# Performance work log

Measured on AMD Instinct MI355X. Metric: run time of the kernel, lower is better.

The kernel has to match this reference:

```python
import jax, jax.numpy as jnp
import numpy as np

N = 100000      # number of vertices
E = 3200000     # number of directed edges (avg degree 32)
EPS = 1e-8
WEIGHT = 0.01


def setup_inputs() -> dict:
    key = jax.random.key(0)
    k1, k2, k3, k4 = jax.random.split(key, 4)
    mu0 = jax.random.normal(k1, (N, 3), dtype=jnp.float32)
    # current positions = canonical + small deformation (realistic ARAP setting)
    mu = mu0 + 0.1 * jax.random.normal(k2, (N, 3), dtype=jnp.float32)
    i = jax.random.randint(k3, (E,), 0, N, dtype=jnp.int32)
    # avoid self-edges (rest length 0 would give w = 1/eps = 1e8 and swamp the loss)
    off = jax.random.randint(k4, (E,), 1, N, dtype=jnp.int32)
    j = (i + off) % N
    edge_idx = jnp.stack([i, j], axis=0)  # (2, E)
    return {"mu0": mu0, "mu": mu, "edge_idx": edge_idx}


def reference(mu0, mu, edge_idx):
    i, j = edge_idx[0], edge_idx[1]
    rest = mu0[j] - mu0[i]        # (E,3) canonical edge vectors
    deform = mu[j] - mu[i]        # (E,3) deformed edge vectors
    w = 1.0 / (jnp.linalg.norm(rest, axis=-1) + EPS)  # (E,)
    # per-edge weighted outer product deform \otimes rest
    outer = jnp.einsum('e,ei,ej->eij', w, deform, rest)  # (E,3,3)
    # scatter-add into per-node covariance matrices
    S = jnp.zeros((mu0.shape[0], 3, 3), dtype=mu0.dtype).at[i].add(outer)  # (N,3,3)
    U, _, Vh = jnp.linalg.svd(S, full_matrices=False)
    R = U @ Vh
    det_mask = (jnp.linalg.det(R) < 0)[:, None, None]
    diag_fix = jnp.array([-1.0, 1.0, 1.0], dtype=mu0.dtype).reshape(1, 1, 3)
    Vh = jnp.where(det_mask, Vh * diag_fix, Vh)
    R = U @ Vh                      # (N,3,3) best-fit rotations
    Ri = R[i]                       # (E,3,3)
    pred = jnp.einsum('eij,ej->ei', Ri, rest)
    err = deform - pred
    loss = jnp.sum(w * jnp.sum(err * err, axis=-1)) / jnp.sum(w)
    return WEIGHT * loss
```

## Files before the change

### kernel.cpp

```cpp
#include <hip/hip_runtime.h>
#include <hip/hip_fp16.h>
#include <math.h>

#define EPS     1e-8f
#define MP      131
#define JBITS   17
#define JMASK   ((1u << JBITS) - 1u)
#define CAP     6144
#define PMAX    1024
#define ACC_T   576
#define MAXPT   11
#define BIN_T   512
#define CHUNK   8192
#define EPT     16

struct alignas(16) Pk { __half2 a, b, c; unsigned pad; };

__global__ __launch_bounds__(256) void k_prep(
    const float* __restrict__ mu0, const float* __restrict__ mu,
    Pk* __restrict__ pk, int* __restrict__ gcursor, int N, int P)
{
    int n = blockIdx.x * blockDim.x + threadIdx.x;
    if (n < P) gcursor[n] = n * CAP;
    if (n >= N) return;
    float x0 = mu0[3*n+0], y0 = mu0[3*n+1], z0 = mu0[3*n+2];
    float x1 = mu [3*n+0], y1 = mu [3*n+1], z1 = mu [3*n+2];
    Pk o;
    o.a = __floats2half2_rn(x0, y0);
    o.b = __floats2half2_rn(z0, x1);
    o.c = __floats2half2_rn(y1, z1);
    o.pad = 0u;
    pk[n] = o;
}

__global__ __launch_bounds__(BIN_T) void k_bin(
    const int* __restrict__ ei, const int* __restrict__ ej,
    int* __restrict__ gcursor, unsigned* __restrict__ bucket,
    int E, int P)
{
    __shared__ int cnt[PMAX];
    __shared__ int dbase[PMAX];
    __shared__ int scan_tmp[PMAX];
    __shared__ unsigned sortw[CHUNK];
    __shared__ unsigned short sortp[CHUNK];

    int lo = blockIdx.x * CHUNK;
    int hi = lo + CHUNK; if (hi > E) hi = E;
    int ce = hi - lo;
    int tid = threadIdx.x;

    for (int t = tid; t < PMAX; t += BIN_T) cnt[t] = 0;

    int myi[EPT], myj[EPT];
    #pragma unroll
    for (int k = 0; k < EPT; ++k) {
        int e = lo + tid + k * BIN_T;
        if (e < hi) {
            myi[k] = __builtin_nontemporal_load(&ei[e]);
            myj[k] = __builtin_nontemporal_load(&ej[e]);
        } else myi[k] = -1;
    }
    __syncthreads();

    #pragma unroll
    for (int k = 0; k < EPT; ++k)
        if (myi[k] >= 0) atomicAdd(&cnt[(unsigned)myi[k] / (unsigned)MP], 1);
    __syncthreads();

    {
        int t1 = tid + BIN_T;
        scan_tmp[tid] = cnt[tid];
        scan_tmp[t1]  = cnt[t1];
        __syncthreads();
        for (int off = 1; off < PMAX; off <<= 1) {
            int a0 = (tid >= off) ? scan_tmp[tid - off] : 0;
            int a1 = scan_tmp[t1 - off];
            __syncthreads();
            scan_tmp[tid] += a0;
            scan_tmp[t1]  += a1;
            __syncthreads();
        }
    }

    for (int t = tid; t < P; t += BIN_T) {
        int c = cnt[t];
        int excl = scan_tmp[t] - c;
        int b = c ? atomicAdd(&gcursor[t], c) : 0;
        dbase[t] = b - excl;
        cnt[t] = excl;
    }
    __syncthreads();

    #pragma unroll
    for (int k = 0; k < EPT; ++k) {
        if (myi[k] >= 0) {
            int i = myi[k];
            int p = (int)((unsigned)i / (unsigned)MP);
            int li = i - p * MP;
            int pos = atomicAdd(&cnt[p], 1);
            sortw[pos] = ((unsigned)li << JBITS) | (unsigned)myj[k];
            sortp[pos] = (unsigned short)p;
        }
    }
    __syncthreads();

    for (int s = tid; s < ce; s += BIN_T) {
        unsigned w = sortw[s];
        int p = sortp[s];
        int dst = dbase[p] + s;
        if (dst < (p + 1) * CAP)
            bucket[dst] = w;
    }
}

__global__ __launch_bounds__(ACC_T) void k_accum(
    const Pk* __restrict__ pk,
    const unsigned* __restrict__ bucket, const int* __restrict__ gcursor,
    double* __restrict__ pblk, int N)
{
    __shared__ unsigned sorted[CAP];
    __shared__ int hist[MP];
    __shared__ int offs[MP];
    __shared__ int cursor[MP];
    __shared__ int sc[192];
    __shared__ float Sl[MP * 9];
    __shared__ double redw[9], rede[9];

    int p = blockIdx.x;
    int lo_n = p * MP;
    int beg = p * CAP;
    int end = gcursor[p];
    int cap_end = beg + CAP;
    if (end > cap_end) end = cap_end;

    for (int t = threadIdx.x; t < MP; t += ACC_T) hist[t] = 0;
    __syncthreads();

    unsigned myu[MAXPT];
    int mycnt = 0;
    {
        int e = beg + threadIdx.x;
        #pragma unroll
        for (int k = 0; k < MAXPT; ++k) {
            if (e < end) {
                unsigned uu = bucket[e];
                myu[k] = uu;
                atomicAdd(&hist[uu >> JBITS], 1);
                ++mycnt;
            }
            e += ACC_T;
        }
    }
    __syncthreads();

    if (threadIdx.x < 192) {
        int v = (threadIdx.x < MP) ? hist[threadIdx.x] : 0;
        int incl = v;
        #pragma unroll
        for (int d = 1; d < 64; d <<= 1) {
            int o = __shfl_up(incl, d);
            if ((threadIdx.x & 63) >= d) incl += o;
        }
        sc[threadIdx.x] = incl;
    }
    __syncthreads();
    if (threadIdx.x < MP) {
        int w = threadIdx.x >> 6;
        int carry = 0;
        if (w >= 1) carry += sc[63];
        if (w >= 2) carry += sc[127];
        int excl = sc[threadIdx.x] - hist[threadIdx.x] + carry;
        offs[threadIdx.x] = excl;
        cursor[threadIdx.x] = excl;
    }
    __syncthreads();

    #pragma unroll
    for (int k = 0; k < MAXPT; ++k) {
        if (k < mycnt) {
            unsigned uu = myu[k];
            int li = (int)(uu >> JBITS);
            int pos = atomicAdd(&cursor[li], 1);
            sorted[pos] = uu;
        }
    }
    __syncthreads();

    double wsum = 0.0, errsum = 0.0;
    float S[9] = {0.f,0.f,0.f,0.f,0.f,0.f,0.f,0.f,0.f};
    {
        int node = threadIdx.x >> 2;
        int part = threadIdx.x & 3;
        int n = lo_n + node;
        if (node < MP && n < N) {
            Pk ac = pk[n];
            float2 a01 = __half22float2(ac.a);
            float2 a23 = __half22float2(ac.b);
            float2 a45 = __half22float2(ac.c);
            float ax = a01.x, ay = a01.y, az = a23.x;
            float cx = a23.y, cy = a45.x, cz = a45.y;

            auto body = [&](const Pk& cc) {
                float2 f01 = __half22float2(cc.a);
                float2 f23 = __half22float2(cc.b);
                float2 f45 = __half22float2(cc.c);
                float r0 = f01.x - ax, r1 = f01.y - ay, r2 = f23.x - az;
                float d0 = f23.y - cx, d1 = f45.x - cy, d2 = f45.y - cz;
                float rr = r0*r0 + r1*r1 + r2*r2;
                float dd = d0*d0 + d1*d1 + d2*d2;
                float w  = 1.0f / (sqrtf(rr) + EPS);
                wsum   += (double)w;
                errsum += (double)(w * (dd + rr));
                float wd0 = w*d0, wd1 = w*d1, wd2 = w*d2;
                S[0] += wd0*r0; S[1] += wd0*r1; S[2] += wd0*r2;
                S[3] += wd1*r0; S[4] += wd1*r1; S[5] += wd1*r2;
                S[6] += wd2*r0; S[7] += wd2*r1; S[8] += wd2*r2;
            };

            int b0 = offs[node];
            int e1 = b0 + hist[node];
            int e  = b0 + part;
            for (; e + 4 < e1; e += 8) {
                unsigned u0 = sorted[e], u1 = sorted[e + 4];
                Pk c0 = pk[u0 & JMASK];
                Pk c1 = pk[u1 & JMASK];
                body(c0);
                body(c1);
            }
            if (e < e1) {
                Pk c0 = pk[sorted[e] & JMASK];
                body(c0);
            }
        }
        #pragma unroll
        for (int c = 0; c < 9; ++c) {
            S[c] += __shfl_down(S[c], 2);
            S[c] += __shfl_down(S[c], 1);
        }
        if (part == 0 && node < MP)
            #pragma unroll
            for (int c = 0; c < 9; ++c) Sl[node*9 + c] = S[c];
    }
    __syncthreads();

    if (threadIdx.x < MP && lo_n + (int)threadIdx.x < N) {
        float Sf[9], X[9];
        #pragma unroll
        for (int c = 0; c < 9; ++c) { Sf[c] = Sl[threadIdx.x*9 + c]; X[c] = Sf[c]; }
        bool ok = true;
        #pragma unroll
        for (int it = 0; it < 8; ++it) {
            float c00 =  (X[4]*X[8] - X[5]*X[7]);
            float c01 = -(X[3]*X[8] - X[5]*X[6]);
            float c02 =  (X[3]*X[7] - X[4]*X[6]);
            float c10 = -(X[1]*X[8] - X[2]*X[7]);
            float c11 =  (X[0]*X[8] - X[2]*X[6]);
            float c12 = -(X[0]*X[7] - X[1]*X[6]);
            float c20 =  (X[1]*X[5] - X[2]*X[4]);
            float c21 = -(X[0]*X[5] - X[2]*X[3]);
            float c22 =  (X[0]*X[4] - X[1]*X[3]);
            float det = X[0]*c00 + X[1]*c01 + X[2]*c02;
            if (!(fabsf(det) > 1e-30f)) { ok = false; break; }
            float inv_det = 1.0f / det;
            float Y[9] = { c00*inv_det, c01*inv_det, c02*inv_det,
                           c10*inv_det, c11*inv_det, c12*inv_det,
                           c20*inv_det, c21*inv_det, c22*inv_det };
            float nx = 0.f, ny = 0.f;
            #pragma unroll
            for (int c = 0; c < 9; ++c) { nx += X[c]*X[c]; ny += Y[c]*Y[c]; }
            float g = sqrtf(sqrtf(ny / nx));
            float hg = 0.5f * g, hig = 0.5f / g;
            #pragma unroll
            for (int c = 0; c < 9; ++c) X[c] = hg * X[c] + hig * Y[c];
        }
        if (!ok) {
            X[0]=1.f; X[1]=0.f; X[2]=0.f;
            X[3]=0.f; X[4]=1.f; X[5]=0.f;
            X[6]=0.f; X[7]=0.f; X[8]=1.f;
        }
        float det = X[0]*(X[4]*X[8] - X[5]*X[7])
                  - X[1]*(X[3]*X[8] - X[5]*X[6])
                  + X[2]*(X[3]*X[7] - X[4]*X[6]);
        if (det < 0.f) { X[0] = -X[0]; X[3] = -X[3]; X[6] = -X[6]; }
        float tr = X[0]*Sf[0] + X[1]*Sf[1] + X[2]*Sf[2]
                 + X[3]*Sf[3] + X[4]*Sf[4] + X[5]*Sf[5]
                 + X[6]*Sf[6] + X[7]*Sf[7] + X[8]*Sf[8];
        errsum -= 2.0 * (double)tr;
    }

    #pragma unroll
    for (int off = 32; off > 0; off >>= 1) {
        wsum   += __shfl_down(wsum, off);
        errsum += __shfl_down(errsum, off);
    }
    if ((threadIdx.x & 63) == 0) {
        redw[threadIdx.x >> 6] = wsum;
        rede[threadIdx.x >> 6] = errsum;
    }
    __syncthreads();
    if (threadIdx.x == 0) {
        double W = 0.0, Er = 0.0;
        #pragma unroll
        for (int k = 0; k < 9; ++k) { W += redw[k]; Er += rede[k]; }
        pblk[2*p]   = W;
        pblk[2*p+1] = Er;
    }
}

__global__ __launch_bounds__(256) void k_final(
    const double* __restrict__ pblk, int nb, float* __restrict__ out)
{
    __shared__ double sw[4], se[4];
    double w = 0.0, e = 0.0;
    for (int t = threadIdx.x; t < nb; t += 256) {
        w += pblk[2*t];
        e += pblk[2*t+1];
    }
    #pragma unroll
    for (int off = 32; off > 0; off >>= 1) {
        w += __shfl_down(w, off);
        e += __shfl_down(e, off);
    }
    if ((threadIdx.x & 63) == 0) {
        sw[threadIdx.x >> 6] = w;
        se[threadIdx.x >> 6] = e;
    }
    __syncthreads();
    if (threadIdx.x == 0) {
        double W  = sw[0] + sw[1] + sw[2] + sw[3];
        double Er = se[0] + se[1] + se[2] + se[3];
        out[0] = (float)(0.01 * (Er / W));
    }
}

extern "C" void kernel_launch(void* const* d_in, const int* in_sizes, int n_in,
                              void* d_out, int out_size, void* d_ws, size_t ws_size,
                              hipStream_t stream) {
    const float* mu0 = (const float*)d_in[0];
    const float* mu  = (const float*)d_in[1];
    const int*   eidx = (const int*)d_in[2];
    int N = in_sizes[0] / 3;
    int E = in_sizes[2] / 2;
    const int* ei = eidx;
    const int* ej = eidx + E;

    int P = (N + MP - 1) / MP;

    double*   pblk    = (double*)d_ws;
    int*      gcursor = (int*)((char*)d_ws + 2 * PMAX * sizeof(double));
    Pk*       pk      = (Pk*)((char*)d_ws + 2 * PMAX * sizeof(double) + PMAX * sizeof(int));
    unsigned* bucket  = (unsigned*)(pk + N);

    int nbin = (E + CHUNK - 1) / CHUNK;

    k_prep  <<<(N + 255) / 256, 256, 0, stream>>>(mu0, mu, pk, gcursor, N, P);
    k_bin   <<<nbin, BIN_T, 0, stream>>>(ei, ej, gcursor, bucket, E, P);
    k_accum <<<P, ACC_T, 0, stream>>>(pk, bucket, gcursor, pblk, N);
    k_final <<<1, 256, 0, stream>>>(pblk, P, (float*)d_out);
}
```

Before: 130.7 us.

## Replace per-block local sort with shared-memory atomic accumulation of covariances

The accumulation kernel no longer builds a per-node histogram, prefix scan and local counting sort of bucketed edges. Each thread now streams edges straight from the bucket array, reads the source node's packed data from a shared-memory cache, and adds the nine weighted outer-product terms into shared per-node matrices with LDS float atomics. This drops several barriers, the sort staging and the register buffers, at the cost of nine shared atomics per edge with possible contention on high-degree nodes. It also makes the float summation order nondeterministic.

```diff
diff --git a/kernel.cpp b/kernel.cpp
--- a/kernel.cpp
+++ b/kernel.cpp
@@ -9,7 +9,6 @@
 #define CAP     6144
 #define PMAX    1024
 #define ACC_T   576
-#define MAXPT   11
 #define BIN_T   512
 #define CHUNK   8192
 #define EPT     16
@@ -118,12 +117,8 @@
     const unsigned* __restrict__ bucket, const int* __restrict__ gcursor,
     double* __restrict__ pblk, int N)
 {
-    __shared__ unsigned sorted[CAP];
-    __shared__ int hist[MP];
-    __shared__ int offs[MP];
-    __shared__ int cursor[MP];
-    __shared__ int sc[192];
     __shared__ float Sl[MP * 9];
+    __shared__ Pk lpk[MP];
     __shared__ double redw[9], rede[9];
 
     int p = blockIdx.x;
@@ -132,121 +127,63 @@
     int end = gcursor[p];
     int cap_end = beg + CAP;
     if (end > cap_end) end = cap_end;
-
-    for (int t = threadIdx.x; t < MP; t += ACC_T) hist[t] = 0;
-    __syncthreads();
-
-    unsigned myu[MAXPT];
-    int mycnt = 0;
-    {
-        int e = beg + threadIdx.x;
-        #pragma unroll
-        for (int k = 0; k < MAXPT; ++k) {
-            if (e < end) {
-                unsigned uu = bucket[e];
-                myu[k] = uu;
-                atomicAdd(&hist[uu >> JBITS], 1);
-                ++mycnt;
-            }
-            e += ACC_T;
-        }
-    }
-    __syncthreads();
-
-    if (threadIdx.x < 192) {
-        int v = (threadIdx.x < MP) ? hist[threadIdx.x] : 0;
-        int incl = v;
-        #pragma unroll
-        for (int d = 1; d < 64; d <<= 1) {
-            int o = __shfl_up(incl, d);
-            if ((threadIdx.x & 63) >= d) incl += o;
-        }
-        sc[threadIdx.x] = incl;
-    }
-    __syncthreads();
-    if (threadIdx.x < MP) {
-        int w = threadIdx.x >> 6;
-        int carry = 0;
-        if (w >= 1) carry += sc[63];
-        if (w >= 2) carry += sc[127];
-        int excl = sc[threadIdx.x] - hist[threadIdx.x] + carry;
-        offs[threadIdx.x] = excl;
-        cursor[threadIdx.x] = excl;
-    }
-    __syncthreads();
-
-    #pragma unroll
-    for (int k = 0; k < MAXPT; ++k) {
-        if (k < mycnt) {
-            unsigned uu = myu[k];
-            int li = (int)(uu >> JBITS);
-            int pos = atomicAdd(&cursor[li], 1);
-            sorted[pos] = uu;
-        }
+    int tid = threadIdx.x;
+
+    for (int t = tid; t < MP * 9; t += ACC_T) Sl[t] = 0.f;
+    for (int t = tid; t < MP; t += ACC_T) {
+        int n = lo_n + t;
+        if (n < N) lpk[t] = pk[n];
     }
     __syncthreads();
 
     double wsum = 0.0, errsum = 0.0;
-    float S[9] = {0.f,0.f,0.f,0.f,0.f,0.f,0.f,0.f,0.f};
-    {
-        int node = threadIdx.x >> 2;
-        int part = threadIdx.x & 3;
-        int n = lo_n + node;
-        if (node < MP && n < N) {
-            Pk ac = pk[n];
-            float2 a01 = __half22float2(ac.a);
-            float2 a23 = __half22float2(ac.b);
-            float2 a45 = __half22float2(ac.c);
-            float ax = a01.x, ay = a01.y, az = a23.x;
-            float cx = a23.y, cy = a45.x, cz = a45.y;
-
-            auto body = [&](const Pk& cc) {
-                float2 f01 = __half22float2(cc.a);
-                float2 f23 = __half22float2(cc.b);
-                float2 f45 = __half22float2(cc.c);
-                float r0 = f01.x - ax, r1 = f01.y - ay, r2 = f23.x - az;
-                float d0 = f23.y - cx, d1 = f45.x - cy, d2 = f45.y - cz;
-                float rr = r0*r0 + r1*r1 + r2*r2;
-                float dd = d0*d0 + d1*d1 + d2*d2;
-                float w  = 1.0f / (sqrtf(rr) + EPS);
-                wsum   += (double)w;
-                errsum += (double)(w * (dd + rr));
-                float wd0 = w*d0, wd1 = w*d1, wd2 = w*d2;
-                S[0] += wd0*r0; S[1] += wd0*r1; S[2] += wd0*r2;
-                S[3] += wd1*r0; S[4] += wd1*r1; S[5] += wd1*r2;
-                S[6] += wd2*r0; S[7] += wd2*r1; S[8] += wd2*r2;
-            };
-
-            int b0 = offs[node];
-            int e1 = b0 + hist[node];
-            int e  = b0 + part;
-            for (; e + 4 < e1; e += 8) {
-                unsigned u0 = sorted[e], u1 = sorted[e + 4];
-                Pk c0 = pk[u0 & JMASK];
-                Pk c1 = pk[u1 & JMASK];
-                body(c0);
-                body(c1);
-            }
-            if (e < e1) {
-                Pk c0 = pk[sorted[e] & JMASK];
-                body(c0);
-            }
-        }
-        #pragma unroll
-        for (int c = 0; c < 9; ++c) {
-            S[c] += __shfl_down(S[c], 2);
-            S[c] += __shfl_down(S[c], 1);
-        }
-        if (part == 0 && node < MP)
-            #pragma unroll
-            for (int c = 0; c < 9; ++c) Sl[node*9 + c] = S[c];
-    }
-    __syncthreads();
-
-    if (threadIdx.x < MP && lo_n + (int)threadIdx.x < N) {
+
+    auto body = [&](unsigned u, const Pk& cc) {
+        int li = (int)(u >> JBITS);
+        Pk ac = lpk[li];
+        float2 a01 = __half22float2(ac.a);
+        float2 a23 = __half22float2(ac.b);
+        float2 a45 = __half22float2(ac.c);
+        float2 f01 = __half22float2(cc.a);
+        float2 f23 = __half22float2(cc.b);
+        float2 f45 = __half22float2(cc.c);
+        float r0 = f01.x - a01.x, r1 = f01.y - a01.y, r2 = f23.x - a23.x;
+        float d0 = f23.y - a23.y, d1 = f45.x - a45.x, d2 = f45.y - a45.y;
+        float rr = r0*r0 + r1*r1 + r2*r2;
+        float dd = d0*d0 + d1*d1 + d2*d2;
+        float w  = 1.0f / (sqrtf(rr) + EPS);
+        wsum   += (double)w;
+        errsum += (double)(w * (dd + rr));
+        float wd0 = w*d0, wd1 = w*d1, wd2 = w*d2;
+        float* s = &Sl[li * 9];
+        atomicAdd(&s[0], wd0*r0); atomicAdd(&s[1], wd0*r1); atomicAdd(&s[2], wd0*r2);
+        atomicAdd(&s[3], wd1*r0); atomicAdd(&s[4], wd1*r1); atomicAdd(&s[5], wd1*r2);
+        atomicAdd(&s[6], wd2*r0); atomicAdd(&s[7], wd2*r1); atomicAdd(&s[8], wd2*r2);
+    };
+
+    int e = beg + tid;
+    for (; e + 3 * ACC_T < end; e += 4 * ACC_T) {
+        unsigned u0 = bucket[e];
+        unsigned u1 = bucket[e +     ACC_T];
+        unsigned u2 = bucket[e + 2 * ACC_T];
+        unsigned u3 = bucket[e + 3 * ACC_T];
+        Pk c0 = pk[u0 & JMASK];
+        Pk c1 = pk[u1 & JMASK];
+        Pk c2 = pk[u2 & JMASK];
+        Pk c3 = pk[u3 & JMASK];
+        body(u0, c0); body(u1, c1); body(u2, c2); body(u3, c3);
+    }
+    for (; e < end; e += ACC_T) {
+        unsigned u = bucket[e];
+        Pk c = pk[u & JMASK];
+        body(u, c);
+    }
+    __syncthreads();
+
+    if (tid < MP && lo_n + tid < N) {
         float Sf[9], X[9];
         #pragma unroll
-        for (int c = 0; c < 9; ++c) { Sf[c] = Sl[threadIdx.x*9 + c]; X[c] = Sf[c]; }
+        for (int c = 0; c < 9; ++c) { Sf[c] = Sl[tid*9 + c]; X[c] = Sf[c]; }
         bool ok = true;
         #pragma unroll
         for (int it = 0; it < 8; ++it) {
@@ -293,12 +230,12 @@
         wsum   += __shfl_down(wsum, off);
         errsum += __shfl_down(errsum, off);
     }
-    if ((threadIdx.x & 63) == 0) {
-        redw[threadIdx.x >> 6] = wsum;
-        rede[threadIdx.x >> 6] = errsum;
-    }
-    __syncthreads();
-    if (threadIdx.x == 0) {
+    if ((tid & 63) == 0) {
+        redw[tid >> 6] = wsum;
+        rede[tid >> 6] = errsum;
+    }
+    __syncthreads();
+    if (tid == 0) {
         double W = 0.0, Er = 0.0;
         #pragma unroll
         for (int k = 0; k < 9; ++k) { W += redw[k]; Er += rede[k]; }
```

Result: slower. 252.7 us (+93.4%).
